# Performance work log

Measured on AMD Instinct MI355X. Metric: run time of the kernel, lower is better.

The kernel has to match this reference:

```python
import jax, jax.numpy as jnp
import numpy as np

# config (matches init_kwargs)
D, H, KV, HD, L, F, V, NC, S = 1024, 16, 4, 64, 6, 4096, 4096, 15, 16
KVD = KV * HD            # 256
ATTN_SCALING = 1.0
EPS = 1e-6
POS = 7                  # current cache write position


def _rms(x, w):
    return x * jax.lax.rsqrt(jnp.mean(x * x, axis=-1, keepdims=True) + EPS) * w


def _rot(x):
    h = x.shape[-1] // 2
    return jnp.concatenate([-x[..., h:], x[..., :h]], axis=-1)


def setup_inputs() -> dict:
    key = jax.random.key(0)
    ks = iter(jax.random.split(key, 24))
    def rn(shape, s):
        return jax.random.normal(next(ks), shape, jnp.float32) * s
    return {
        "input_embeds": rn((1, D, 1, 1), 1.0),
        "cache_length": POS,
        "key_cache": rn((1, L * KVD, 1, S), 0.5),
        "key_padding_mask": jnp.where(jnp.arange(S) <= POS, 0.0, -1e9)[None, :].astype(jnp.float32),
        "kv_cache_update_mask": (jnp.arange(S) == POS).astype(jnp.float32)[None, :],
        "value_cache": rn((1, L * KVD, 1, S), 0.5),
        "inv_freq": 1.0 / (10000.0 ** (jnp.arange(0, HD, 2, dtype=jnp.float32) / HD)),
        "Wq": rn((L, H * HD, D), 0.02),
        "Wk": rn((L, KVD, D), 0.02),
        "Wv": rn((L, KVD, D), 0.02),
        "Wo": rn((L, D, H * HD), 0.02),
        "ln1_w": jnp.ones((L, D), jnp.float32),
        "ln2_w": jnp.ones((L, D), jnp.float32),
        "qn_w": jnp.ones((L, HD), jnp.float32),
        "kn_w": jnp.ones((L, HD), jnp.float32),
        "Wgate": rn((L, F, D), 0.02),
        "Wup": rn((L, F, D), 0.02),
        "Wdown": rn((L, D, F), 0.02),
        "norm_w": jnp.ones((D,), jnp.float32),
        "lm_head_w": rn((NC, V, D), 0.02),
    }


def _forward(input_embeds, key_cache, key_padding_mask, kv_cache_update_mask,
             value_cache, inv_freq, Wq, Wk, Wv, Wo, ln1_w, ln2_w, qn_w, kn_w,
             Wgate, Wup, Wdown, norm_w, lm_head_w, cache_length):
    pos = jnp.asarray(cache_length, jnp.float32)
    freqs = inv_freq * pos                       # [HD/2]
    emb = jnp.concatenate([freqs, freqs])        # [HD]
    cos = jnp.cos(emb) * ATTN_SCALING
    sin = jnp.sin(emb) * ATTN_SCALING
    umask = kv_cache_update_mask[0]              # [S]
    pmask = key_padding_mask[0]                  # [S]
    kcache = key_cache.reshape(L, KVD, S)
    vcache = value_cache.reshape(L, KVD, S)
    hidden0 = input_embeds.reshape(D)
    n_rep = H // KV
    scale = 1.0 / (HD ** 0.5)

    def layer(hidden, p):
        Wq_, Wk_, Wv_, Wo_, ln1, ln2, qn, kn, Wg_, Wu_, Wd_, kc_l, vc_l = p
        h = _rms(hidden, ln1)
        q = _rms((Wq_ @ h).reshape(H, HD), qn)   # [H,HD]
        k = _rms((Wk_ @ h).reshape(KV, HD), kn)  # [KV,HD]
        v = (Wv_ @ h).reshape(KV, HD)
        q = q * cos + _rot(q) * sin
        k = k * cos + _rot(k) * sin
        nk = k.reshape(KVD)
        nv = v.reshape(KVD)
        # masked scatter-write into this layer's cache slice
        kc = kc_l * (1.0 - umask) + nk[:, None] * umask   # [KVD,S]
        vc = vc_l * (1.0 - umask) + nv[:, None] * umask
        kc = jnp.repeat(kc.reshape(KV, HD, S), n_rep, axis=0)  # GQA expand -> [H,HD,S]
        vc = jnp.repeat(vc.reshape(KV, HD, S), n_rep, axis=0)
        scores = jnp.einsum('hd,hds->hs', q, kc) * scale + pmask  # [H,S]
        aw = jax.nn.softmax(scores, axis=-1)
        ao = jnp.einsum('hs,hds->hd', aw, vc).reshape(H * HD)
        hidden = hidden + Wo_ @ ao
        h = _rms(hidden, ln2)
        hidden = hidden + Wd_ @ (jax.nn.silu(Wg_ @ h) * (Wu_ @ h))
        return hidden, (nk, nv)

    hidden, (nks, nvs) = jax.lax.scan(
        layer, hidden0,
        (Wq, Wk, Wv, Wo, ln1_w, ln2_w, qn_w, kn_w, Wgate, Wup, Wdown, kcache, vcache))

    normed = _rms(hidden, norm_w)                          # [D]
    all_logits = jnp.einsum('nvd,d->nv', lm_head_w, normed)[None]  # [1,NC,V]
    hidden_out = normed.reshape(1, D, 1, 1)
    um4 = kv_cache_update_mask[:, None, None, :]           # [1,1,1,S]
    new_k = nks.reshape(1, L * KVD, 1, 1)
    new_v = nvs.reshape(1, L * KVD, 1, 1)
    nkc = key_cache * (1.0 - um4) + new_k * um4
    nvc = value_cache * (1.0 - um4) + new_v * um4
    return (all_logits, hidden_out, nkc, nvc)


def reference(input_embeds, cache_length, key_cache, key_padding_mask,
              kv_cache_update_mask, value_cache, inv_freq, Wq, Wk, Wv, Wo,
              ln1_w, ln2_w, qn_w, kn_w, Wgate, Wup, Wdown, norm_w, lm_head_w):
    return _forward(input_embeds, key_cache, key_padding_mask, kv_cache_update_mask,
                    value_cache, inv_freq, Wq, Wk, Wv, Wo, ln1_w, ln2_w, qn_w, kn_w,
                    Wgate, Wup, Wdown, norm_w, lm_head_w, cache_length)
```

## Files before the change

kernel.cpp:

```cpp
#include <hip/hip_runtime.h>

#define DD     1024
#define HH     16
#define KVH    4
#define HDIM   64
#define NLAYER 6
#define FDIM   4096
#define VDIM   4096
#define NCODE  15
#define SS     16
#define KVDIM  256
#define EPSF   1e-6f

__device__ __forceinline__ float dot4(float4 a, float4 b){
  return a.x*b.x + a.y*b.y + a.z*b.z + a.w*b.w;
}
__device__ __forceinline__ float wave_sum(float v){
  #pragma unroll
  for (int o=32;o;o>>=1) v += __shfl_xor(v,o);
  return v;
}
__device__ __forceinline__ float grp16_sum(float v){
  #pragma unroll
  for (int o=8;o;o>>=1) v += __shfl_xor(v,o);
  return v;
}
__device__ __forceinline__ float grp16_max(float v){
  #pragma unroll
  for (int o=8;o;o>>=1) v = fmaxf(v, __shfl_xor(v,o));
  return v;
}

__global__ __launch_bounds__(256) void k_init(const float* __restrict__ emb,
                                              float* __restrict__ hidden){
  ((float4*)hidden)[threadIdx.x] = ((const float4*)emb)[threadIdx.x];
}

__global__ __launch_bounds__(256) void k_qkv(
    const float* __restrict__ Wq, const float* __restrict__ Wk, const float* __restrict__ Wv,
    const float* __restrict__ hidden, const float* __restrict__ ln,
    float* __restrict__ out )
{
  __shared__ float xs[DD];
  __shared__ float red[4];
  const int t = threadIdx.x, lane = t & 63, wid = t >> 6;
  float4 hv = ((const float4*)hidden)[t];
  float ss = wave_sum(dot4(hv,hv));
  if (lane==0) red[wid] = ss;
  __syncthreads();
  const float inv = rsqrtf((red[0]+red[1]+red[2]+red[3])*(1.0f/DD) + EPSF);
  float4 lw = ((const float4*)ln)[t];
  float4 xv; xv.x=hv.x*inv*lw.x; xv.y=hv.y*inv*lw.y; xv.z=hv.z*inv*lw.z; xv.w=hv.w*inv*lw.w;
  ((float4*)xs)[t] = xv;
  __syncthreads();
  const int row = blockIdx.x*4 + wid;
  const float* Wrow;
  if (row < 1024)      Wrow = Wq + (size_t)row*DD;
  else if (row < 1280) Wrow = Wk + (size_t)(row-1024)*DD;
  else                 Wrow = Wv + (size_t)(row-1280)*DD;
  const float4* w4 = (const float4*)Wrow;
  const float4* x4 = (const float4*)xs;
  float acc = 0.f;
  #pragma unroll
  for (int j=0;j<4;j++) acc += dot4(w4[j*64+lane], x4[j*64+lane]);
  acc = wave_sum(acc);
  if (lane==0) out[row] = acc;
}

__global__ __launch_bounds__(256) void k_attn(
    const float* __restrict__ qbuf, const float* __restrict__ kbuf, const float* __restrict__ vbuf,
    const float* __restrict__ qn, const float* __restrict__ kn,
    const float* __restrict__ inv_freq, const int* __restrict__ cache_len,
    const float* __restrict__ kcache_l, const float* __restrict__ vcache_l,
    const float* __restrict__ pmask, const float* __restrict__ umask,
    float* __restrict__ ao, float* __restrict__ knew, float* __restrict__ vnew)
{
  __shared__ float qsh[DD];
  __shared__ float ksh[KVDIM];
  __shared__ float vsh[KVDIM];
  __shared__ float awsh[HH*SS];
  __shared__ float umsh[SS], pmsh[SS];
  const int t = threadIdx.x;
  if (t < SS){ umsh[t]=umask[t]; pmsh[t]=pmask[t]; }
  const float pos = (float)cache_len[0];

  {
    const int idx16 = t & 15;
    float4 q = ((const float4*)qbuf)[t];
    float ss = grp16_sum(dot4(q,q));
    const float inv = rsqrtf(ss*(1.0f/HDIM)+EPSF);
    float4 w = ((const float4*)qn)[idx16];
    float x0=q.x*inv*w.x, x1=q.y*inv*w.y, x2=q.z*inv*w.z, x3=q.w*inv*w.w;
    float p0=__shfl_xor(x0,8), p1=__shfl_xor(x1,8), p2=__shfl_xor(x2,8), p3=__shfl_xor(x3,8);
    const int d0 = idx16*4;
    const bool lolane = (idx16 < 8);
    const int m = lolane ? d0 : d0-32;
    const float f0=inv_freq[m]*pos, f1=inv_freq[m+1]*pos, f2=inv_freq[m+2]*pos, f3=inv_freq[m+3]*pos;
    const float sgn = lolane ? -1.f : 1.f;
    float4 r;
    r.x = x0*cosf(f0) + sgn*p0*sinf(f0);
    r.y = x1*cosf(f1) + sgn*p1*sinf(f1);
    r.z = x2*cosf(f2) + sgn*p2*sinf(f2);
    r.w = x3*cosf(f3) + sgn*p3*sinf(f3);
    ((float4*)qsh)[t] = r;
  }
  if (t < 64){
    const int idx16 = t & 15;
    float4 k = ((const float4*)kbuf)[t];
    float ss = grp16_sum(dot4(k,k));
    const float inv = rsqrtf(ss*(1.0f/HDIM)+EPSF);
    float4 w = ((const float4*)kn)[idx16];
    float x0=k.x*inv*w.x, x1=k.y*inv*w.y, x2=k.z*inv*w.z, x3=k.w*inv*w.w;
    float p0=__shfl_xor(x0,8), p1=__shfl_xor(x1,8), p2=__shfl_xor(x2,8), p3=__shfl_xor(x3,8);
    const int d0 = idx16*4;
    const bool lolane = (idx16 < 8);
    const int m = lolane ? d0 : d0-32;
    const float f0=inv_freq[m]*pos, f1=inv_freq[m+1]*pos, f2=inv_freq[m+2]*pos, f3=inv_freq[m+3]*pos;
    const float sgn = lolane ? -1.f : 1.f;
    float4 r;
    r.x = x0*cosf(f0) + sgn*p0*sinf(f0);
    r.y = x1*cosf(f1) + sgn*p1*sinf(f1);
    r.z = x2*cosf(f2) + sgn*p2*sinf(f2);
    r.w = x3*cosf(f3) + sgn*p3*sinf(f3);
    ((float4*)ksh)[t] = r;
    ((float4*)knew)[t] = r;
    float4 v = ((const float4*)vbuf)[t];
    ((float4*)vsh)[t] = v;
    ((float4*)vnew)[t] = v;
  }
  __syncthreads();
  {
    const int h = t>>4, s = t&15, kvh = h>>2;
    const float um = umsh[s], pm = pmsh[s];
    const float* kcol = kcache_l + (size_t)(kvh*HDIM)*SS + s;
    const float* ksrc = ksh + kvh*HDIM;
    const float* qv   = qsh + h*HDIM;
    float dot = 0.f;
    #pragma unroll
    for (int d=0; d<HDIM; d++){
      float kc = kcol[d*SS]*(1.f-um) + ksrc[d]*um;
      dot += qv[d]*kc;
    }
    const float sc = dot*0.125f + pm;
    const float mx = grp16_max(sc);
    const float e  = expf(sc-mx);
    const float sm = grp16_sum(e);
    awsh[t] = e/sm;
  }
  __syncthreads();
  {
    const int h = t>>4, idx16 = t&15, kvh = h>>2;
    const int cb = kvh*HDIM + idx16*4;
    float a0=0,a1=0,a2=0,a3=0;
    #pragma unroll
    for (int s=0;s<SS;s++){
      const float aw = awsh[h*16+s];
      const float um = umsh[s];
      a0 += aw*(vcache_l[(size_t)(cb+0)*SS+s]*(1.f-um)+vsh[cb+0]*um);
      a1 += aw*(vcache_l[(size_t)(cb+1)*SS+s]*(1.f-um)+vsh[cb+1]*um);
      a2 += aw*(vcache_l[(size_t)(cb+2)*SS+s]*(1.f-um)+vsh[cb+2]*um);
      a3 += aw*(vcache_l[(size_t)(cb+3)*SS+s]*(1.f-um)+vsh[cb+3]*um);
    }
    ((float4*)ao)[t] = make_float4(a0,a1,a2,a3);
  }
}

__global__ __launch_bounds__(256) void k_o(
    const float* __restrict__ Wo, const float* __restrict__ ao, float* __restrict__ hidden)
{
  __shared__ float xs[DD];
  const int t=threadIdx.x, lane=t&63, wid=t>>6;
  ((float4*)xs)[t] = ((const float4*)ao)[t];
  __syncthreads();
  const int row = blockIdx.x*4 + wid;
  const float4* w4 = (const float4*)(Wo + (size_t)row*DD);
  const float4* x4 = (const float4*)xs;
  float acc=0.f;
  #pragma unroll
  for (int j=0;j<4;j++) acc += dot4(w4[j*64+lane], x4[j*64+lane]);
  acc = wave_sum(acc);
  if (lane==0) hidden[row] += acc;
}

__global__ __launch_bounds__(256) void k_gu(
    const float* __restrict__ Wg, const float* __restrict__ Wu,
    const float* __restrict__ hidden, const float* __restrict__ ln,
    float* __restrict__ act)
{
  __shared__ float xs[DD];
  __shared__ float red[4];
  const int t=threadIdx.x, lane=t&63, wid=t>>6;
  float4 hv = ((const float4*)hidden)[t];
  float ss = wave_sum(dot4(hv,hv));
  if (lane==0) red[wid]=ss;
  __syncthreads();
  const float inv = rsqrtf((red[0]+red[1]+red[2]+red[3])*(1.0f/DD) + EPSF);
  float4 lw = ((const float4*)ln)[t];
  float4 xv; xv.x=hv.x*inv*lw.x; xv.y=hv.y*inv*lw.y; xv.z=hv.z*inv*lw.z; xv.w=hv.w*inv*lw.w;
  ((float4*)xs)[t] = xv;
  __syncthreads();
  const int row = blockIdx.x*4 + wid;
  const float4* g4 = (const float4*)(Wg + (size_t)row*DD);
  const float4* u4 = (const float4*)(Wu + (size_t)row*DD);
  const float4* x4 = (const float4*)xs;
  float ag=0.f, au=0.f;
  #pragma unroll
  for (int j=0;j<4;j++){
    float4 x = x4[j*64+lane];
    ag += dot4(g4[j*64+lane], x);
    au += dot4(u4[j*64+lane], x);
  }
  ag = wave_sum(ag); au = wave_sum(au);
  if (lane==0){
    float sg = ag/(1.f+expf(-ag));
    act[row] = sg*au;
  }
}

__global__ __launch_bounds__(256) void k_down(
    const float* __restrict__ Wd, const float* __restrict__ act, float* __restrict__ hidden)
{
  __shared__ float xs[FDIM];
  const int t=threadIdx.x, lane=t&63, wid=t>>6;
  #pragma unroll
  for (int j=0;j<4;j++) ((float4*)xs)[j*256+t] = ((const float4*)act)[j*256+t];
  __syncthreads();
  const int row = blockIdx.x*4 + wid;
  const float4* w4 = (const float4*)(Wd + (size_t)row*FDIM);
  const float4* x4 = (const float4*)xs;
  float acc=0.f;
  #pragma unroll
  for (int j=0;j<16;j++) acc += dot4(w4[j*64+lane], x4[j*64+lane]);
  acc = wave_sum(acc);
  if (lane==0) hidden[row] += acc;
}

__global__ __launch_bounds__(256) void k_finalize(
    const float* __restrict__ hidden, const float* __restrict__ norm_w,
    const float* __restrict__ kcache, const float* __restrict__ vcache,
    const float* __restrict__ knew, const float* __restrict__ vnew,
    const float* __restrict__ umask,
    float* __restrict__ normed, float* __restrict__ out_hidden,
    float* __restrict__ out_nkc, float* __restrict__ out_nvc)
{
  if (blockIdx.x == 0){
    __shared__ float red[4];
    const int t=threadIdx.x, lane=t&63, wid=t>>6;
    float4 hv = ((const float4*)hidden)[t];
    float ss = wave_sum(dot4(hv,hv));
    if (lane==0) red[wid]=ss;
    __syncthreads();
    const float inv = rsqrtf((red[0]+red[1]+red[2]+red[3])*(1.0f/DD) + EPSF);
    float4 w = ((const float4*)norm_w)[t];
    float4 nv; nv.x=hv.x*inv*w.x; nv.y=hv.y*inv*w.y; nv.z=hv.z*inv*w.z; nv.w=hv.w*inv*w.w;
    ((float4*)normed)[t]   = nv;
    ((float4*)out_hidden)[t] = nv;
  } else {
    const int j = (blockIdx.x-1)*256 + threadIdx.x;
    if (j < NLAYER*KVDIM*SS){
      const int s = j & 15, c = j >> 4;
      const float um = umask[s];
      out_nkc[j] = kcache[j]*(1.f-um) + knew[c]*um;
    } else {
      const int i = j - NLAYER*KVDIM*SS;
      const int s = i & 15, c = i >> 4;
      const float um = umask[s];
      out_nvc[i] = vcache[i]*(1.f-um) + vnew[c]*um;
    }
  }
}

__global__ __launch_bounds__(256) void k_lmhead(
    const float* __restrict__ W, const float* __restrict__ normed, float* __restrict__ out)
{
  __shared__ float xs[DD];
  const int t=threadIdx.x, lane=t&63, wid=t>>6;
  ((float4*)xs)[t] = ((const float4*)normed)[t];
  __syncthreads();
  const int row = blockIdx.x*4 + wid;
  const float4* w4 = (const float4*)(W + (size_t)row*DD);
  const float4* x4 = (const float4*)xs;
  float acc=0.f;
  #pragma unroll
  for (int j=0;j<4;j++) acc += dot4(w4[j*64+lane], x4[j*64+lane]);
  acc = wave_sum(acc);
  if (lane==0) out[row] = acc;
}

extern "C" void kernel_launch(void* const* d_in, const int* in_sizes, int n_in,
                              void* d_out, int out_size, void* d_ws, size_t ws_size,
                              hipStream_t stream)
{
  const float* emb    = (const float*)d_in[0];
  const int*   clen   = (const int*)  d_in[1];
  const float* kcache = (const float*)d_in[2];
  const float* pmask  = (const float*)d_in[3];
  const float* umask  = (const float*)d_in[4];
  const float* vcache = (const float*)d_in[5];
  const float* invf   = (const float*)d_in[6];
  const float* Wq     = (const float*)d_in[7];
  const float* Wk     = (const float*)d_in[8];
  const float* Wv     = (const float*)d_in[9];
  const float* Wo     = (const float*)d_in[10];
  const float* ln1    = (const float*)d_in[11];
  const float* ln2    = (const float*)d_in[12];
  const float* qn     = (const float*)d_in[13];
  const float* kn     = (const float*)d_in[14];
  const float* Wg     = (const float*)d_in[15];
  const float* Wu     = (const float*)d_in[16];
  const float* Wd     = (const float*)d_in[17];
  const float* nw     = (const float*)d_in[18];
  const float* lmw    = (const float*)d_in[19];
  float* out = (float*)d_out;
  float* ws  = (float*)d_ws;

  float* hidden = ws;
  float* qkv    = ws + 1024;
  float* ao     = ws + 2560;
  float* act    = ws + 3584;
  float* knew   = ws + 7680;
  float* vnew   = ws + 9216;
  float* normed = ws + 10752;

  float* out_logits = out;
  float* out_hidden = out + NCODE*VDIM;
  float* out_nkc    = out_hidden + DD;
  float* out_nvc    = out_nkc + NLAYER*KVDIM*SS;

  k_init<<<1,256,0,stream>>>(emb, hidden);
  for (int l=0; l<NLAYER; l++){
    k_qkv<<<384,256,0,stream>>>(Wq + (size_t)l*HH*HDIM*DD, Wk + (size_t)l*KVDIM*DD,
                                Wv + (size_t)l*KVDIM*DD, hidden, ln1 + l*DD, qkv);
    k_attn<<<1,256,0,stream>>>(qkv, qkv+1024, qkv+1280, qn + l*HDIM, kn + l*HDIM,
                               invf, clen,
                               kcache + (size_t)l*KVDIM*SS, vcache + (size_t)l*KVDIM*SS,
                               pmask, umask, ao, knew + l*KVDIM, vnew + l*KVDIM);
    k_o<<<256,256,0,stream>>>(Wo + (size_t)l*DD*HH*HDIM, ao, hidden);
    k_gu<<<1024,256,0,stream>>>(Wg + (size_t)l*FDIM*DD, Wu + (size_t)l*FDIM*DD,
                                hidden, ln2 + l*DD, act);
    k_down<<<256,256,0,stream>>>(Wd + (size_t)l*DD*FDIM, act, hidden);
  }
  k_finalize<<<193,256,0,stream>>>(hidden, nw, kcache, vcache, knew, vnew, umask,
                                   normed, out_hidden, out_nkc, out_nvc);
  k_lmhead<<<15360,256,0,stream>>>(lmw, normed, out_logits);
}
```

Baseline: 682.3 us.

## Fuse whole decode into one persistent cooperative kernel with grid syncs

Replaces the per-layer chain of separate kernel launches with a single cooperative kernel of 256 blocks by 1024 threads. Grid-wide syncs separate the QKV, attention+O-proj, gate/up and down phases. Each block redundantly computes attention locally so O-proj needs no extra grid sync, and the final norm, KV cache merge and LM head also run inside the kernel. The aim is to remove launch overhead and inter-kernel gaps, at the cost of grid.sync latency, duplicated attention work per block, and exposure to blocks that finish unevenly.

```diff
diff --git a/kernel.cpp b/kernel.cpp
--- a/kernel.cpp
+++ b/kernel.cpp
@@ -1,4 +1,6 @@
 #include <hip/hip_runtime.h>
+#include <hip/hip_cooperative_groups.h>
+namespace cg = cooperative_groups;
 
 #define DD     1024
 #define HH     16
@@ -31,316 +33,288 @@
   return v;
 }
 
-__global__ __launch_bounds__(256) void k_init(const float* __restrict__ emb,
-                                              float* __restrict__ hidden){
-  ((float4*)hidden)[threadIdx.x] = ((const float4*)emb)[threadIdx.x];
-}
-
-__global__ __launch_bounds__(256) void k_qkv(
-    const float* __restrict__ Wq, const float* __restrict__ Wk, const float* __restrict__ Wv,
-    const float* __restrict__ hidden, const float* __restrict__ ln,
-    float* __restrict__ out )
+struct KP {
+  const float *emb, *kcache, *pmask, *umask, *vcache, *invf;
+  const float *Wq, *Wk, *Wv, *Wo, *ln1, *ln2, *qn, *kn, *Wg, *Wu, *Wd, *nw, *lmw;
+  const int   *clen;
+  float *hidden, *qkv, *act, *knew, *vnew;
+  float *out_logits, *out_hidden, *out_nkc, *out_nvc;
+};
+
+__global__ __launch_bounds__(1024) void k_decode(KP p)
 {
-  __shared__ float xs[DD];
-  __shared__ float red[4];
-  const int t = threadIdx.x, lane = t & 63, wid = t >> 6;
-  float4 hv = ((const float4*)hidden)[t];
-  float ss = wave_sum(dot4(hv,hv));
-  if (lane==0) red[wid] = ss;
-  __syncthreads();
-  const float inv = rsqrtf((red[0]+red[1]+red[2]+red[3])*(1.0f/DD) + EPSF);
-  float4 lw = ((const float4*)ln)[t];
-  float4 xv; xv.x=hv.x*inv*lw.x; xv.y=hv.y*inv*lw.y; xv.z=hv.z*inv*lw.z; xv.w=hv.w*inv*lw.w;
-  ((float4*)xs)[t] = xv;
-  __syncthreads();
-  const int row = blockIdx.x*4 + wid;
-  const float* Wrow;
-  if (row < 1024)      Wrow = Wq + (size_t)row*DD;
-  else if (row < 1280) Wrow = Wk + (size_t)(row-1024)*DD;
-  else                 Wrow = Wv + (size_t)(row-1280)*DD;
-  const float4* w4 = (const float4*)Wrow;
-  const float4* x4 = (const float4*)xs;
-  float acc = 0.f;
-  #pragma unroll
-  for (int j=0;j<4;j++) acc += dot4(w4[j*64+lane], x4[j*64+lane]);
-  acc = wave_sum(acc);
-  if (lane==0) out[row] = acc;
-}
-
-__global__ __launch_bounds__(256) void k_attn(
-    const float* __restrict__ qbuf, const float* __restrict__ kbuf, const float* __restrict__ vbuf,
-    const float* __restrict__ qn, const float* __restrict__ kn,
-    const float* __restrict__ inv_freq, const int* __restrict__ cache_len,
-    const float* __restrict__ kcache_l, const float* __restrict__ vcache_l,
-    const float* __restrict__ pmask, const float* __restrict__ umask,
-    float* __restrict__ ao, float* __restrict__ knew, float* __restrict__ vnew)
-{
+  cg::grid_group grid = cg::this_grid();
+  const int t    = threadIdx.x;
+  const int b    = blockIdx.x;
+  const int lane = t & 63, wid = t >> 6;
+  const int gw   = (b << 4) + wid;
+
+  __shared__ float xs[FDIM];
   __shared__ float qsh[DD];
-  __shared__ float ksh[KVDIM];
-  __shared__ float vsh[KVDIM];
+  __shared__ float aosh[DD];
+  __shared__ float ksh[KVDIM], vsh[KVDIM];
   __shared__ float awsh[HH*SS];
   __shared__ float umsh[SS], pmsh[SS];
-  const int t = threadIdx.x;
-  if (t < SS){ umsh[t]=umask[t]; pmsh[t]=pmask[t]; }
-  const float pos = (float)cache_len[0];
+  __shared__ float red[16];
+
+  const float pos = (float)p.clen[0];
+
+  #pragma unroll 1
+  for (int l = 0; l < NLAYER; l++){
+    const float* Wq_l = p.Wq + (size_t)l*DD*DD;
+    const float* Wk_l = p.Wk + (size_t)l*KVDIM*DD;
+    const float* Wv_l = p.Wv + (size_t)l*KVDIM*DD;
+    const float* Wo_l = p.Wo + (size_t)l*DD*DD;
+    const float* Wg_l = p.Wg + (size_t)l*FDIM*DD;
+    const float* Wu_l = p.Wu + (size_t)l*FDIM*DD;
+    const float* Wd_l = p.Wd + (size_t)l*DD*FDIM;
+    const float* kc_l = p.kcache + (size_t)l*KVDIM*SS;
+    const float* vc_l = p.vcache + (size_t)l*KVDIM*SS;
+    const float* hsrc = (l == 0) ? p.emb : p.hidden;
+
+    {
+      float hv = hsrc[t];
+      float ss = wave_sum(hv*hv);
+      if (lane == 0) red[wid] = ss;
+      __syncthreads();
+      float tot = 0.f;
+      #pragma unroll
+      for (int i=0;i<16;i++) tot += red[i];
+      const float inv = rsqrtf(tot*(1.0f/DD) + EPSF);
+      xs[t] = hv*inv*p.ln1[l*DD + t];
+      __syncthreads();
+    }
+    if (gw < 1536){
+      const float* Wrow = (gw < 1024) ? Wq_l + (size_t)gw*DD
+                        : (gw < 1280) ? Wk_l + (size_t)(gw-1024)*DD
+                                      : Wv_l + (size_t)(gw-1280)*DD;
+      const float4* w4 = (const float4*)Wrow;
+      const float4* x4 = (const float4*)xs;
+      float acc = 0.f;
+      #pragma unroll
+      for (int j=0;j<4;j++) acc += dot4(w4[j*64+lane], x4[j*64+lane]);
+      acc = wave_sum(acc);
+      if (lane == 0) p.qkv[gw] = acc;
+    }
+    grid.sync();
+
+    if (t < SS){ umsh[t] = p.umask[t]; pmsh[t] = p.pmask[t]; }
+    if (t < 256){
+      const int idx16 = t & 15;
+      float4 q = ((const float4*)p.qkv)[t];
+      float ss = grp16_sum(dot4(q,q));
+      const float inv = rsqrtf(ss*(1.0f/HDIM) + EPSF);
+      float4 w = ((const float4*)(p.qn + l*HDIM))[idx16];
+      float x0=q.x*inv*w.x, x1=q.y*inv*w.y, x2=q.z*inv*w.z, x3=q.w*inv*w.w;
+      float p0=__shfl_xor(x0,8), p1=__shfl_xor(x1,8), p2=__shfl_xor(x2,8), p3=__shfl_xor(x3,8);
+      const int d0 = idx16*4;
+      const bool lolane = (idx16 < 8);
+      const int m = lolane ? d0 : d0-32;
+      const float f0=p.invf[m]*pos, f1=p.invf[m+1]*pos, f2=p.invf[m+2]*pos, f3=p.invf[m+3]*pos;
+      const float sgn = lolane ? -1.f : 1.f;
+      float4 r;
+      r.x = x0*cosf(f0) + sgn*p0*sinf(f0);
+      r.y = x1*cosf(f1) + sgn*p1*sinf(f1);
+      r.z = x2*cosf(f2) + sgn*p2*sinf(f2);
+      r.w = x3*cosf(f3) + sgn*p3*sinf(f3);
+      ((float4*)qsh)[t] = r;
+    }
+    if (t < 64){
+      const int idx16 = t & 15;
+      float4 k = ((const float4*)(p.qkv + 1024))[t];
+      float ss = grp16_sum(dot4(k,k));
+      const float inv = rsqrtf(ss*(1.0f/HDIM) + EPSF);
+      float4 w = ((const float4*)(p.kn + l*HDIM))[idx16];
+      float x0=k.x*inv*w.x, x1=k.y*inv*w.y, x2=k.z*inv*w.z, x3=k.w*inv*w.w;
+      float p0=__shfl_xor(x0,8), p1=__shfl_xor(x1,8), p2=__shfl_xor(x2,8), p3=__shfl_xor(x3,8);
+      const int d0 = idx16*4;
+      const bool lolane = (idx16 < 8);
+      const int m = lolane ? d0 : d0-32;
+      const float f0=p.invf[m]*pos, f1=p.invf[m+1]*pos, f2=p.invf[m+2]*pos, f3=p.invf[m+3]*pos;
+      const float sgn = lolane ? -1.f : 1.f;
+      float4 r;
+      r.x = x0*cosf(f0) + sgn*p0*sinf(f0);
+      r.y = x1*cosf(f1) + sgn*p1*sinf(f1);
+      r.z = x2*cosf(f2) + sgn*p2*sinf(f2);
+      r.w = x3*cosf(f3) + sgn*p3*sinf(f3);
+      ((float4*)ksh)[t] = r;
+      float4 v = ((const float4*)(p.qkv + 1280))[t];
+      ((float4*)vsh)[t] = v;
+      if (b == 0){
+        ((float4*)(p.knew + l*KVDIM))[t] = r;
+        ((float4*)(p.vnew + l*KVDIM))[t] = v;
+      }
+    }
+    __syncthreads();
+    if (t < 256){
+      const int h = t>>4, s = t&15, kvh = h>>2;
+      const float um = umsh[s], pm = pmsh[s];
+      const float* kcol = kc_l + (size_t)(kvh*HDIM)*SS + s;
+      const float* ksrc = ksh + kvh*HDIM;
+      const float* qv   = qsh + h*HDIM;
+      float dot = 0.f;
+      #pragma unroll
+      for (int d=0; d<HDIM; d++){
+        float kc = kcol[d*SS]*(1.f-um) + ksrc[d]*um;
+        dot += qv[d]*kc;
+      }
+      const float sc = dot*0.125f + pm;
+      const float mx = grp16_max(sc);
+      const float e  = expf(sc-mx);
+      const float sm = grp16_sum(e);
+      awsh[t] = e/sm;
+    }
+    __syncthreads();
+    if (t < 256){
+      const int h = t>>4, idx16 = t&15, kvh = h>>2;
+      const int cb = kvh*HDIM + idx16*4;
+      float a0=0,a1=0,a2=0,a3=0;
+      #pragma unroll
+      for (int s=0;s<SS;s++){
+        const float aw = awsh[h*16+s];
+        const float um = umsh[s];
+        a0 += aw*(vc_l[(size_t)(cb+0)*SS+s]*(1.f-um)+vsh[cb+0]*um);
+        a1 += aw*(vc_l[(size_t)(cb+1)*SS+s]*(1.f-um)+vsh[cb+1]*um);
+        a2 += aw*(vc_l[(size_t)(cb+2)*SS+s]*(1.f-um)+vsh[cb+2]*um);
+        a3 += aw*(vc_l[(size_t)(cb+3)*SS+s]*(1.f-um)+vsh[cb+3]*um);
+      }
+      ((float4*)aosh)[t] = make_float4(a0,a1,a2,a3);
+    }
+    __syncthreads();
+    if (gw < 1024){
+      const float4* w4 = (const float4*)(Wo_l + (size_t)gw*DD);
+      const float4* x4 = (const float4*)aosh;
+      float acc = 0.f;
+      #pragma unroll
+      for (int j=0;j<4;j++) acc += dot4(w4[j*64+lane], x4[j*64+lane]);
+      acc = wave_sum(acc);
+      if (lane == 0) p.hidden[gw] = hsrc[gw] + acc;
+    }
+    grid.sync();
+
+    {
+      float hv = p.hidden[t];
+      float ss = wave_sum(hv*hv);
+      if (lane == 0) red[wid] = ss;
+      __syncthreads();
+      float tot = 0.f;
+      #pragma unroll
+      for (int i=0;i<16;i++) tot += red[i];
+      const float inv = rsqrtf(tot*(1.0f/DD) + EPSF);
+      xs[t] = hv*inv*p.ln2[l*DD + t];
+      __syncthreads();
+    }
+    {
+      const float4* g4 = (const float4*)(Wg_l + (size_t)gw*DD);
+      const float4* u4 = (const float4*)(Wu_l + (size_t)gw*DD);
+      const float4* x4 = (const float4*)xs;
+      float ag=0.f, au=0.f;
+      #pragma unroll
+      for (int j=0;j<4;j++){
+        float4 x = x4[j*64+lane];
+        ag += dot4(g4[j*64+lane], x);
+        au += dot4(u4[j*64+lane], x);
+      }
+      ag = wave_sum(ag); au = wave_sum(au);
+      if (lane == 0) p.act[gw] = (ag/(1.f+expf(-ag)))*au;
+    }
+    grid.sync();
+
+    ((float4*)xs)[t] = ((const float4*)p.act)[t];
+    __syncthreads();
+    if (gw < 1024){
+      const float4* w4 = (const float4*)(Wd_l + (size_t)gw*FDIM);
+      const float4* x4 = (const float4*)xs;
+      float acc = 0.f;
+      #pragma unroll
+      for (int j=0;j<16;j++) acc += dot4(w4[j*64+lane], x4[j*64+lane]);
+      acc = wave_sum(acc);
+      if (lane == 0) p.hidden[gw] += acc;
+    }
+    grid.sync();
+  }
 
   {
-    const int idx16 = t & 15;
-    float4 q = ((const float4*)qbuf)[t];
-    float ss = grp16_sum(dot4(q,q));
-    const float inv = rsqrtf(ss*(1.0f/HDIM)+EPSF);
-    float4 w = ((const float4*)qn)[idx16];
-    float x0=q.x*inv*w.x, x1=q.y*inv*w.y, x2=q.z*inv*w.z, x3=q.w*inv*w.w;
-    float p0=__shfl_xor(x0,8), p1=__shfl_xor(x1,8), p2=__shfl_xor(x2,8), p3=__shfl_xor(x3,8);
-    const int d0 = idx16*4;
-    const bool lolane = (idx16 < 8);
-    const int m = lolane ? d0 : d0-32;
-    const float f0=inv_freq[m]*pos, f1=inv_freq[m+1]*pos, f2=inv_freq[m+2]*pos, f3=inv_freq[m+3]*pos;
-    const float sgn = lolane ? -1.f : 1.f;
-    float4 r;
-    r.x = x0*cosf(f0) + sgn*p0*sinf(f0);
-    r.y = x1*cosf(f1) + sgn*p1*sinf(f1);
-    r.z = x2*cosf(f2) + sgn*p2*sinf(f2);
-    r.w = x3*cosf(f3) + sgn*p3*sinf(f3);
-    ((float4*)qsh)[t] = r;
+    float hv = p.hidden[t];
+    float ss = wave_sum(hv*hv);
+    if (lane == 0) red[wid] = ss;
+    __syncthreads();
+    float tot = 0.f;
+    #pragma unroll
+    for (int i=0;i<16;i++) tot += red[i];
+    const float inv = rsqrtf(tot*(1.0f/DD) + EPSF);
+    xs[t] = hv*inv*p.nw[t];
+    __syncthreads();
   }
-  if (t < 64){
-    const int idx16 = t & 15;
-    float4 k = ((const float4*)kbuf)[t];
-    float ss = grp16_sum(dot4(k,k));
-    const float inv = rsqrtf(ss*(1.0f/HDIM)+EPSF);
-    float4 w = ((const float4*)kn)[idx16];
-    float x0=k.x*inv*w.x, x1=k.y*inv*w.y, x2=k.z*inv*w.z, x3=k.w*inv*w.w;
-    float p0=__shfl_xor(x0,8), p1=__shfl_xor(x1,8), p2=__shfl_xor(x2,8), p3=__shfl_xor(x3,8);
-    const int d0 = idx16*4;
-    const bool lolane = (idx16 < 8);
-    const int m = lolane ? d0 : d0-32;
-    const float f0=inv_freq[m]*pos, f1=inv_freq[m+1]*pos, f2=inv_freq[m+2]*pos, f3=inv_freq[m+3]*pos;
-    const float sgn = lolane ? -1.f : 1.f;
-    float4 r;
-    r.x = x0*cosf(f0) + sgn*p0*sinf(f0);
-    r.y = x1*cosf(f1) + sgn*p1*sinf(f1);
-    r.z = x2*cosf(f2) + sgn*p2*sinf(f2);
-    r.w = x3*cosf(f3) + sgn*p3*sinf(f3);
-    ((float4*)ksh)[t] = r;
-    ((float4*)knew)[t] = r;
-    float4 v = ((const float4*)vbuf)[t];
-    ((float4*)vsh)[t] = v;
-    ((float4*)vnew)[t] = v;
-  }
-  __syncthreads();
-  {
-    const int h = t>>4, s = t&15, kvh = h>>2;
-    const float um = umsh[s], pm = pmsh[s];
-    const float* kcol = kcache_l + (size_t)(kvh*HDIM)*SS + s;
-    const float* ksrc = ksh + kvh*HDIM;
-    const float* qv   = qsh + h*HDIM;
-    float dot = 0.f;
-    #pragma unroll
-    for (int d=0; d<HDIM; d++){
-      float kc = kcol[d*SS]*(1.f-um) + ksrc[d]*um;
-      dot += qv[d]*kc;
-    }
-    const float sc = dot*0.125f + pm;
-    const float mx = grp16_max(sc);
-    const float e  = expf(sc-mx);
-    const float sm = grp16_sum(e);
-    awsh[t] = e/sm;
-  }
-  __syncthreads();
-  {
-    const int h = t>>4, idx16 = t&15, kvh = h>>2;
-    const int cb = kvh*HDIM + idx16*4;
-    float a0=0,a1=0,a2=0,a3=0;
-    #pragma unroll
-    for (int s=0;s<SS;s++){
-      const float aw = awsh[h*16+s];
-      const float um = umsh[s];
-      a0 += aw*(vcache_l[(size_t)(cb+0)*SS+s]*(1.f-um)+vsh[cb+0]*um);
-      a1 += aw*(vcache_l[(size_t)(cb+1)*SS+s]*(1.f-um)+vsh[cb+1]*um);
-      a2 += aw*(vcache_l[(size_t)(cb+2)*SS+s]*(1.f-um)+vsh[cb+2]*um);
-      a3 += aw*(vcache_l[(size_t)(cb+3)*SS+s]*(1.f-um)+vsh[cb+3]*um);
-    }
-    ((float4*)ao)[t] = make_float4(a0,a1,a2,a3);
-  }
-}
-
-__global__ __launch_bounds__(256) void k_o(
-    const float* __restrict__ Wo, const float* __restrict__ ao, float* __restrict__ hidden)
-{
-  __shared__ float xs[DD];
-  const int t=threadIdx.x, lane=t&63, wid=t>>6;
-  ((float4*)xs)[t] = ((const float4*)ao)[t];
-  __syncthreads();
-  const int row = blockIdx.x*4 + wid;
-  const float4* w4 = (const float4*)(Wo + (size_t)row*DD);
-  const float4* x4 = (const float4*)xs;
-  float acc=0.f;
-  #pragma unroll
-  for (int j=0;j<4;j++) acc += dot4(w4[j*64+lane], x4[j*64+lane]);
-  acc = wave_sum(acc);
-  if (lane==0) hidden[row] += acc;
-}
-
-__global__ __launch_bounds__(256) void k_gu(
-    const float* __restrict__ Wg, const float* __restrict__ Wu,
-    const float* __restrict__ hidden, const float* __restrict__ ln,
-    float* __restrict__ act)
-{
-  __shared__ float xs[DD];
-  __shared__ float red[4];
-  const int t=threadIdx.x, lane=t&63, wid=t>>6;
-  float4 hv = ((const float4*)hidden)[t];
-  float ss = wave_sum(dot4(hv,hv));
-  if (lane==0) red[wid]=ss;
-  __syncthreads();
-  const float inv = rsqrtf((red[0]+red[1]+red[2]+red[3])*(1.0f/DD) + EPSF);
-  float4 lw = ((const float4*)ln)[t];
-  float4 xv; xv.x=hv.x*inv*lw.x; xv.y=hv.y*inv*lw.y; xv.z=hv.z*inv*lw.z; xv.w=hv.w*inv*lw.w;
-  ((float4*)xs)[t] = xv;
-  __syncthreads();
-  const int row = blockIdx.x*4 + wid;
-  const float4* g4 = (const float4*)(Wg + (size_t)row*DD);
-  const float4* u4 = (const float4*)(Wu + (size_t)row*DD);
-  const float4* x4 = (const float4*)xs;
-  float ag=0.f, au=0.f;
-  #pragma unroll
-  for (int j=0;j<4;j++){
-    float4 x = x4[j*64+lane];
-    ag += dot4(g4[j*64+lane], x);
-    au += dot4(u4[j*64+lane], x);
-  }
-  ag = wave_sum(ag); au = wave_sum(au);
-  if (lane==0){
-    float sg = ag/(1.f+expf(-ag));
-    act[row] = sg*au;
-  }
-}
-
-__global__ __launch_bounds__(256) void k_down(
-    const float* __restrict__ Wd, const float* __restrict__ act, float* __restrict__ hidden)
-{
-  __shared__ float xs[FDIM];
-  const int t=threadIdx.x, lane=t&63, wid=t>>6;
-  #pragma unroll
-  for (int j=0;j<4;j++) ((float4*)xs)[j*256+t] = ((const float4*)act)[j*256+t];
-  __syncthreads();
-  const int row = blockIdx.x*4 + wid;
-  const float4* w4 = (const float4*)(Wd + (size_t)row*FDIM);
-  const float4* x4 = (const float4*)xs;
-  float acc=0.f;
-  #pragma unroll
-  for (int j=0;j<16;j++) acc += dot4(w4[j*64+lane], x4[j*64+lane]);
-  acc = wave_sum(acc);
-  if (lane==0) hidden[row] += acc;
-}
-
-__global__ __launch_bounds__(256) void k_finalize(
-    const float* __restrict__ hidden, const float* __restrict__ norm_w,
-    const float* __restrict__ kcache, const float* __restrict__ vcache,
-    const float* __restrict__ knew, const float* __restrict__ vnew,
-    const float* __restrict__ umask,
-    float* __restrict__ normed, float* __restrict__ out_hidden,
-    float* __restrict__ out_nkc, float* __restrict__ out_nvc)
-{
-  if (blockIdx.x == 0){
-    __shared__ float red[4];
-    const int t=threadIdx.x, lane=t&63, wid=t>>6;
-    float4 hv = ((const float4*)hidden)[t];
-    float ss = wave_sum(dot4(hv,hv));
-    if (lane==0) red[wid]=ss;
-    __syncthreads();
-    const float inv = rsqrtf((red[0]+red[1]+red[2]+red[3])*(1.0f/DD) + EPSF);
-    float4 w = ((const float4*)norm_w)[t];
-    float4 nv; nv.x=hv.x*inv*w.x; nv.y=hv.y*inv*w.y; nv.z=hv.z*inv*w.z; nv.w=hv.w*inv*w.w;
-    ((float4*)normed)[t]   = nv;
-    ((float4*)out_hidden)[t] = nv;
-  } else {
-    const int j = (blockIdx.x-1)*256 + threadIdx.x;
+  if (b == 0) p.out_hidden[t] = xs[t];
+  if (t < 192){
+    const int j = b*192 + t;
     if (j < NLAYER*KVDIM*SS){
       const int s = j & 15, c = j >> 4;
-      const float um = umask[s];
-      out_nkc[j] = kcache[j]*(1.f-um) + knew[c]*um;
+      const float um = p.umask[s];
+      p.out_nkc[j] = p.kcache[j]*(1.f-um) + p.knew[c]*um;
     } else {
       const int i = j - NLAYER*KVDIM*SS;
       const int s = i & 15, c = i >> 4;
-      const float um = umask[s];
-      out_nvc[i] = vcache[i]*(1.f-um) + vnew[c]*um;
+      const float um = p.umask[s];
+      p.out_nvc[i] = p.vcache[i]*(1.f-um) + p.vnew[c]*um;
     }
   }
-}
-
-__global__ __launch_bounds__(256) void k_lmhead(
-    const float* __restrict__ W, const float* __restrict__ normed, float* __restrict__ out)
-{
-  __shared__ float xs[DD];
-  const int t=threadIdx.x, lane=t&63, wid=t>>6;
-  ((float4*)xs)[t] = ((const float4*)normed)[t];
-  __syncthreads();
-  const int row = blockIdx.x*4 + wid;
-  const float4* w4 = (const float4*)(W + (size_t)row*DD);
-  const float4* x4 = (const float4*)xs;
-  float acc=0.f;
-  #pragma unroll
-  for (int j=0;j<4;j++) acc += dot4(w4[j*64+lane], x4[j*64+lane]);
-  acc = wave_sum(acc);
-  if (lane==0) out[row] = acc;
+  {
+    const float4* x4 = (const float4*)xs;
+    #pragma unroll 1
+    for (int k=0;k<NCODE;k++){
+      const int row = k*4096 + gw;
+      const float4* w4 = (const float4*)(p.lmw + (size_t)row*DD);
+      float acc = 0.f;
+      #pragma unroll
+      for (int j=0;j<4;j++) acc += dot4(w4[j*64+lane], x4[j*64+lane]);
+      acc = wave_sum(acc);
+      if (lane == 0) p.out_logits[row] = acc;
+    }
+  }
 }
 
 extern "C" void kernel_launch(void* const* d_in, const int* in_sizes, int n_in,
                               void* d_out, int out_size, void* d_ws, size_t ws_size,
                               hipStream_t stream)
 {
-  const float* emb    = (const float*)d_in[0];
-  const int*   clen   = (const int*)  d_in[1];
-  const float* kcache = (const float*)d_in[2];
-  const float* pmask  = (const float*)d_in[3];
-  const float* umask  = (const float*)d_in[4];
-  const float* vcache = (const float*)d_in[5];
-  const float* invf   = (const float*)d_in[6];
-  const float* Wq     = (const float*)d_in[7];
-  const float* Wk     = (const float*)d_in[8];
-  const float* Wv     = (const float*)d_in[9];
-  const float* Wo     = (const float*)d_in[10];
-  const float* ln1    = (const float*)d_in[11];
-  const float* ln2    = (const float*)d_in[12];
-  const float* qn     = (const float*)d_in[13];
-  const float* kn     = (const float*)d_in[14];
-  const float* Wg     = (const float*)d_in[15];
-  const float* Wu     = (const float*)d_in[16];
-  const float* Wd     = (const float*)d_in[17];
-  const float* nw     = (const float*)d_in[18];
-  const float* lmw    = (const float*)d_in[19];
+  KP hp;
+  hp.emb    = (const float*)d_in[0];
+  hp.clen   = (const int*)  d_in[1];
+  hp.kcache = (const float*)d_in[2];
+  hp.pmask  = (const float*)d_in[3];
+  hp.umask  = (const float*)d_in[4];
+  hp.vcache = (const float*)d_in[5];
+  hp.invf   = (const float*)d_in[6];
+  hp.Wq     = (const float*)d_in[7];
+  hp.Wk     = (const float*)d_in[8];
+  hp.Wv     = (const float*)d_in[9];
+  hp.Wo     = (const float*)d_in[10];
+  hp.ln1    = (const float*)d_in[11];
+  hp.ln2    = (const float*)d_in[12];
+  hp.qn     = (const float*)d_in[13];
+  hp.kn     = (const float*)d_in[14];
+  hp.Wg     = (const float*)d_in[15];
+  hp.Wu     = (const float*)d_in[16];
+  hp.Wd     = (const float*)d_in[17];
+  hp.nw     = (const float*)d_in[18];
+  hp.lmw    = (const float*)d_in[19];
+
+  float* ws = (float*)d_ws;
+  hp.hidden = ws;
+  hp.qkv    = ws + 1024;
+  hp.act    = ws + 2560;
+  hp.knew   = ws + 6656;
+  hp.vnew   = ws + 8192;
+
   float* out = (float*)d_out;
-  float* ws  = (float*)d_ws;
-
-  float* hidden = ws;
-  float* qkv    = ws + 1024;
-  float* ao     = ws + 2560;
-  float* act    = ws + 3584;
-  float* knew   = ws + 7680;
-  float* vnew   = ws + 9216;
-  float* normed = ws + 10752;
-
-  float* out_logits = out;
-  float* out_hidden = out + NCODE*VDIM;
-  float* out_nkc    = out_hidden + DD;
-  float* out_nvc    = out_nkc + NLAYER*KVDIM*SS;
-
-  k_init<<<1,256,0,stream>>>(emb, hidden);
-  for (int l=0; l<NLAYER; l++){
-    k_qkv<<<384,256,0,stream>>>(Wq + (size_t)l*HH*HDIM*DD, Wk + (size_t)l*KVDIM*DD,
-                                Wv + (size_t)l*KVDIM*DD, hidden, ln1 + l*DD, qkv);
-    k_attn<<<1,256,0,stream>>>(qkv, qkv+1024, qkv+1280, qn + l*HDIM, kn + l*HDIM,
-                               invf, clen,
-                               kcache + (size_t)l*KVDIM*SS, vcache + (size_t)l*KVDIM*SS,
-                               pmask, umask, ao, knew + l*KVDIM, vnew + l*KVDIM);
-    k_o<<<256,256,0,stream>>>(Wo + (size_t)l*DD*HH*HDIM, ao, hidden);
-    k_gu<<<1024,256,0,stream>>>(Wg + (size_t)l*FDIM*DD, Wu + (size_t)l*FDIM*DD,
-                                hidden, ln2 + l*DD, act);
-    k_down<<<256,256,0,stream>>>(Wd + (size_t)l*DD*FDIM, act, hidden);
-  }
-  k_finalize<<<193,256,0,stream>>>(hidden, nw, kcache, vcache, knew, vnew, umask,
-                                   normed, out_hidden, out_nkc, out_nvc);
-  k_lmhead<<<15360,256,0,stream>>>(lmw, normed, out_logits);
-}
+  hp.out_logits = out;
+  hp.out_hidden = out + NCODE*VDIM;
+  hp.out_nkc    = hp.out_hidden + DD;
+  hp.out_nvc    = hp.out_nkc + NLAYER*KVDIM*SS;
+
+  void* args[] = { &hp };
+  hipLaunchCooperativeKernel((const void*)k_decode, dim3(256), dim3(1024),
+                             args, 0, stream);
+}
```

New measurement: 1.482 ms. +117.2%, slower.
